# Optimization experiments

Measured on AMD Instinct MI355X. Metric: run time of the kernel, lower is better.

The kernel has to match this reference:

```python
import jax, jax.numpy as jnp
import numpy as np

C_IN = 512
C_MID = 256   # in_channels // ratio
ATTN_CH = 32  # SelectiveKernelAttn attn_channels
NUM_PATHS = 2
BN_EPS = 1e-5
LN_EPS = 1e-5


def conv1x1(x, w, b=None):
    # x: [B,C,H,W], w: [O,C] -> [B,O,H,W]
    y = jnp.einsum('oc,bchw->bohw', w, x)
    if b is not None:
        y = y + b[None, :, None, None]
    return y


def setup_inputs() -> dict:
    key = jax.random.key(0)
    ks = jax.random.split(key, 10)
    B, H, W = 16, 64, 64
    s = 0.05
    return {
        'x': jax.random.normal(ks[0], (B, C_IN, H, W), jnp.float32),
        # channel ('ch') branch params
        'w_qr': jax.random.normal(ks[1], (1, C_IN), jnp.float32) * s,
        'b_qr': jnp.zeros((1,), jnp.float32),
        'w_vr': jax.random.normal(ks[2], (C_MID, C_IN), jnp.float32) * s,
        'b_vr': jnp.zeros((C_MID,), jnp.float32),
        'w_up': jax.random.normal(ks[3], (C_IN, C_MID), jnp.float32) * s,
        'b_up': jnp.zeros((C_IN,), jnp.float32),
        'ln_g': jnp.ones((C_IN,), jnp.float32),
        'ln_b': jnp.zeros((C_IN,), jnp.float32),
        # spatial ('sp') branch params
        'w_ql': jax.random.normal(ks[4], (C_MID, C_IN), jnp.float32) * s,
        'b_ql': jnp.zeros((C_MID,), jnp.float32),
        'w_vl': jax.random.normal(ks[5], (C_MID, C_IN), jnp.float32) * s,
        'b_vl': jnp.zeros((C_MID,), jnp.float32),
        # SelectiveKernelAttn params (fc_reduce, bn eval stats, fc_select)
        'w_red': jax.random.normal(ks[6], (ATTN_CH, C_IN), jnp.float32) * s,
        'bn_g': jnp.ones((ATTN_CH,), jnp.float32),
        'bn_b': jnp.zeros((ATTN_CH,), jnp.float32),
        'bn_rm': jnp.zeros((ATTN_CH,), jnp.float32),
        'bn_rv': jnp.ones((ATTN_CH,), jnp.float32),
        'w_sel': jax.random.normal(ks[7], (C_IN * NUM_PATHS, ATTN_CH), jnp.float32) * s,
    }


def reference(x, w_qr, b_qr, w_vr, b_vr, w_up, b_up, ln_g, ln_b,
              w_ql, b_ql, w_vl, b_vl, w_red, bn_g, bn_b, bn_rm, bn_rv, w_sel):
    B, C, H, W = x.shape
    HW = H * W

    # ---- channel attention ('ch') ----
    input_x = conv1x1(x, w_vr, b_vr).reshape(B, C_MID, HW)            # [B,m,HW]
    mask = jax.nn.softmax(conv1x1(x, w_qr, b_qr).reshape(B, HW), axis=1)  # [B,HW]
    context = jnp.einsum('bmh,bh->bm', input_x, mask)                  # [B,m]
    up = jnp.einsum('om,bm->bo', w_up, context) + b_up                 # [B,C]
    mu = jnp.mean(up, axis=1, keepdims=True)
    var = jnp.var(up, axis=1, keepdims=True)
    ln = (up - mu) * jax.lax.rsqrt(var + LN_EPS) * ln_g + ln_b
    channel_attn = jax.nn.sigmoid(ln)                                  # [B,C]

    # ---- spatial attention ('sp') ----
    g_x = conv1x1(x, w_ql, b_ql)                                       # [B,m,H,W]
    avg = jax.nn.softmax(g_x.max(axis=(2, 3)), axis=1)                 # [B,m]
    theta = conv1x1(x, w_vl, b_vl).reshape(B, C_MID, HW)               # [B,m,HW]
    ctx = jnp.einsum('bm,bmh->bh', avg, theta)                         # [B,HW]
    spatial_attn = jax.nn.softmax(ctx, axis=1)                         # [B,HW]

    # ---- dsa fusion ----
    sequence = (channel_attn[:, :, None] * spatial_attn[:, None, :]).reshape(B, C, H, W)
    parallel = (channel_attn[:, :, None] + spatial_attn[:, None, :]).reshape(B, C, H, W)
    stack = jnp.stack([sequence, parallel], axis=1)                    # [B,2,C,H,W]

    # SelectiveKernelAttn (BN in eval mode with running stats)
    s = stack.sum(axis=1).mean(axis=(2, 3))                            # [B,C]
    red = jnp.einsum('ac,bc->ba', w_red, s)                            # [B,attn]
    red = (red - bn_rm) * jax.lax.rsqrt(bn_rv + BN_EPS) * bn_g + bn_b
    red = jax.nn.relu(red)
    sel = jnp.einsum('oa,ba->bo', w_sel, red).reshape(B, NUM_PATHS, C)
    sk_attn = jax.nn.softmax(sel, axis=1)                              # [B,2,C]

    sq_pr = (stack * sk_attn[:, :, :, None, None]).sum(axis=1)         # [B,C,H,W]
    return x * sq_pr + x
```

## Files before the change

kernel.cpp:

```cpp
#include <hip/hip_runtime.h>
#include <hip/hip_bf16.h>

#define BATCH 16
#define CIN   512
#define CMID  256
#define HWN   4096

typedef __bf16 bf16x8  __attribute__((ext_vector_type(8)));
typedef float  floatx4 __attribute__((ext_vector_type(4)));
typedef int    intx4   __attribute__((ext_vector_type(4)));

__device__ __forceinline__ unsigned short f2bf(float f){
  union { float f; unsigned int u; } v; v.f = f;
  unsigned int u = v.u;
  unsigned int r = u + 0x7FFFu + ((u >> 16) & 1u);
  return (unsigned short)(r >> 16);
}

__device__ __forceinline__ float wred(float v){
  #pragma unroll
  for (int o = 32; o >= 1; o >>= 1) v += __shfl_xor(v, o, 64);
  return v;
}

__device__ __forceinline__ float bsum(float v, float* scr, int t){
  v = wred(v);
  __syncthreads();
  if ((t & 63) == 0) scr[t >> 6] = v;
  __syncthreads();
  return scr[0] + scr[1] + scr[2] + scr[3];
}

__device__ __forceinline__ float bmax(float v, float* scr, int t){
  #pragma unroll
  for (int o = 32; o >= 1; o >>= 1) v = fmaxf(v, __shfl_xor(v, o, 64));
  __syncthreads();
  if ((t & 63) == 0) scr[t >> 6] = v;
  __syncthreads();
  return fmaxf(fmaxf(scr[0], scr[1]), fmaxf(scr[2], scr[3]));
}

__global__ __launch_bounds__(256) void k0_convert(const float* __restrict__ w,
                                                  unsigned short* __restrict__ wbf){
  int i = blockIdx.x * 256 + threadIdx.x;
  wbf[i] = f2bf(w[i]);
}

__global__ __launch_bounds__(256) void k1_gemm(
    const float* __restrict__ x, const unsigned short* __restrict__ wbf,
    const float* __restrict__ w_qr, float* __restrict__ qr, float* __restrict__ gpart)
{
  __shared__ __align__(16) unsigned short Blds[2][64 * 32];
  __shared__ float wqr_s[CIN];

  const int t = threadIdx.x;
  const int ntile = blockIdx.x, b = blockIdx.y;
  const int n0 = ntile * 64;
  const int lane = t & 63, wave = t >> 6, quad = lane >> 4, lm = lane & 15;
  const int n_own = t >> 2, q_own = t & 3;
  const int wblk = (n_own * 4 + (q_own ^ (n_own & 3))) * 8;

  wqr_s[t] = w_qr[t];
  wqr_s[t + 256] = w_qr[t + 256];
  __syncthreads();

  const float* xb = x + (size_t)b * CIN * HWN + (size_t)(q_own * 8) * HWN + n0 + n_own;

  floatx4 acc[4][4];
  #pragma unroll
  for (int i = 0; i < 4; ++i)
    #pragma unroll
    for (int jj = 0; jj < 4; ++jj)
      acc[i][jj] = (floatx4){0.f, 0.f, 0.f, 0.f};

  float qa = 0.f;
  float xv[8];
  bf16x8 afc[4], afn[4];

  #pragma unroll
  for (int j = 0; j < 8; ++j) xv[j] = xb[(size_t)j * HWN];
  #pragma unroll
  for (int j = 0; j < 8; ++j) qa = fmaf(wqr_s[q_own * 8 + j], xv[j], qa);
  {
    union { unsigned short u[8]; intx4 v; } pk;
    #pragma unroll
    for (int j = 0; j < 8; ++j) pk.u[j] = f2bf(xv[j]);
    *(intx4*)(&Blds[0][wblk]) = pk.v;
  }
  #pragma unroll
  for (int ms = 0; ms < 4; ++ms)
    afc[ms] = *(const bf16x8*)(&wbf[(size_t)(wave * 64 + ms * 16 + lm) * CIN + quad * 8]);
  __syncthreads();

  #pragma unroll 2
  for (int kt = 0; kt < 16; ++kt){
    const int cur = kt & 1;
    if (kt < 15){
      #pragma unroll
      for (int j = 0; j < 8; ++j) xv[j] = xb[(size_t)((kt + 1) * 32 + j) * HWN];
      #pragma unroll
      for (int ms = 0; ms < 4; ++ms)
        afn[ms] = *(const bf16x8*)(&wbf[(size_t)(wave * 64 + ms * 16 + lm) * CIN +
                                        (kt + 1) * 32 + quad * 8]);
    }
    bf16x8 bfr[4];
    #pragma unroll
    for (int ns = 0; ns < 4; ++ns){
      const int n = ns * 16 + lm;
      bfr[ns] = *(const bf16x8*)(&Blds[cur][(n * 4 + (quad ^ (n & 3))) * 8]);
    }
    #pragma unroll
    for (int ms = 0; ms < 4; ++ms)
      #pragma unroll
      for (int ns = 0; ns < 4; ++ns)
        acc[ms][ns] = __builtin_amdgcn_mfma_f32_16x16x32_bf16(afc[ms], bfr[ns], acc[ms][ns], 0, 0, 0);
    if (kt < 15){
      #pragma unroll
      for (int j = 0; j < 8; ++j)
        qa = fmaf(wqr_s[(kt + 1) * 32 + q_own * 8 + j], xv[j], qa);
      union { unsigned short u[8]; intx4 v; } pk;
      #pragma unroll
      for (int j = 0; j < 8; ++j) pk.u[j] = f2bf(xv[j]);
      *(intx4*)(&Blds[1 - cur][wblk]) = pk.v;
      #pragma unroll
      for (int ms = 0; ms < 4; ++ms) afc[ms] = afn[ms];
    }
    __syncthreads();
  }

  qa += __shfl_xor(qa, 1, 64);
  qa += __shfl_xor(qa, 2, 64);
  if ((t & 3) == 0) qr[b * HWN + n0 + n_own] = qa;

  #pragma unroll
  for (int ms = 0; ms < 4; ++ms){
    #pragma unroll
    for (int r = 0; r < 4; ++r){
      float v = fmaxf(fmaxf(acc[ms][0][r], acc[ms][1][r]),
                      fmaxf(acc[ms][2][r], acc[ms][3][r]));
      v = fmaxf(v, __shfl_xor(v, 1, 64));
      v = fmaxf(v, __shfl_xor(v, 2, 64));
      v = fmaxf(v, __shfl_xor(v, 4, 64));
      v = fmaxf(v, __shfl_xor(v, 8, 64));
      if ((lane & 15) == 0){
        const int m = wave * 64 + ms * 16 + (lane >> 4) * 4 + r;
        gpart[((b * 64 + ntile) * CMID) + m] = v;
      }
    }
  }
}

__global__ __launch_bounds__(256) void kr1_gmax(
    const float* __restrict__ gpart, const float* __restrict__ b_ql,
    float* __restrict__ gmax)
{
  __shared__ float part[8][32];
  const int b = blockIdx.x, g = blockIdx.y, t = threadIdx.x;
  const int m_l = t & 31, ng = t >> 5;
  const int m = g * 32 + m_l;
  float v = -3.0e38f;
  #pragma unroll
  for (int i = 0; i < 8; ++i)
    v = fmaxf(v, gpart[(size_t)(b * 64 + ng * 8 + i) * CMID + m]);
  part[ng][m_l] = v;
  __syncthreads();
  if (t < 32){
    float mx = part[0][t];
    #pragma unroll
    for (int i = 1; i < 8; ++i) mx = fmaxf(mx, part[i][t]);
    gmax[b * CMID + g * 32 + t] = mx + b_ql[g * 32 + t];
  }
}

__global__ __launch_bounds__(256) void kr2_prep(
    const float* __restrict__ gmax, const float* __restrict__ w_vl,
    const float* __restrict__ qr,
    float* __restrict__ wmix, float* __restrict__ stats,
    float* __restrict__ xmask, float* __restrict__ ctx)
{
  __shared__ float scr[4];
  __shared__ float avg_s[CMID];
  __shared__ float wsum[2][128];
  const int b = blockIdx.x, cg = blockIdx.y, t = threadIdx.x;

  if (cg < 4){
    ((floatx4*)(ctx + (size_t)b * HWN + cg * 1024))[t] = (floatx4){0.f,0.f,0.f,0.f};

    float gv = gmax[b * CMID + t];
    float mx = bmax(gv, scr, t);
    float e = expf(gv - mx);
    float s = bsum(e, scr, t);
    avg_s[t] = e / s;
    __syncthreads();

    const int c = cg * 128 + (t & 127);
    const int half = t >> 7;
    float acc = 0.f;
    #pragma unroll 8
    for (int mi = 0; mi < 128; ++mi){
      const int m = half * 128 + mi;
      acc = fmaf(w_vl[(size_t)m * CIN + c], avg_s[m], acc);
    }
    wsum[half][t & 127] = acc;
    __syncthreads();
    if (t < 128) wmix[b * CIN + cg * 128 + t] = wsum[0][t] + wsum[1][t];
  } else {
    xmask[b * CIN + t] = 0.f;
    xmask[b * CIN + t + 256] = 0.f;
    const float* qb = qr + (size_t)b * HWN;
    float qm = -3.0e38f;
    #pragma unroll
    for (int i = 0; i < 16; ++i) qm = fmaxf(qm, qb[t + i * 256]);
    qm = bmax(qm, scr, t);
    float qs = 0.f;
    #pragma unroll
    for (int i = 0; i < 16; ++i) qs += expf(qb[t + i * 256] - qm);
    qs = bsum(qs, scr, t);
    if (t == 0){ stats[b] = qm; stats[16 + b] = qs; }
  }
}

__global__ __launch_bounds__(256) void k3_dual(
    const float* __restrict__ x, const float* __restrict__ qr,
    const float* __restrict__ stats, const float* __restrict__ wmix,
    float* __restrict__ xmask, float* __restrict__ ctx)
{
  const int ht = blockIdx.x, ct = blockIdx.y, b = blockIdx.z;
  const int t = threadIdx.x;
  const int j = t & 15, i = t >> 4;
  const int c0 = ct * 128, h0 = ht * 128;
  const float* xb = x + (size_t)b * CIN * HWN;
  const float qm = stats[b], inv_qs = 1.0f / stats[16 + b];

  floatx4 maskv[2];
  #pragma unroll
  for (int l = 0; l < 2; ++l)
    #pragma unroll
    for (int d = 0; d < 4; ++d)
      maskv[l][d] = expf(qr[b*HWN + h0 + j*4 + d + 64*l] - qm) * inv_qs;

  float wmv[8];
  #pragma unroll
  for (int k = 0; k < 8; ++k)
    wmv[k] = wmix[b*CIN + c0 + i + 16*k];

  float xm[8] = {0,0,0,0,0,0,0,0};
  floatx4 cx[2];
  cx[0] = (floatx4){0.f,0.f,0.f,0.f};
  cx[1] = (floatx4){0.f,0.f,0.f,0.f};

  #pragma unroll
  for (int k = 0; k < 8; ++k){
    const float* row = xb + (size_t)(c0 + i + 16*k) * HWN + h0 + j*4;
    floatx4 v0 = *(const floatx4*)(row);
    floatx4 v1 = *(const floatx4*)(row + 64);
    floatx4 p = v0 * maskv[0] + v1 * maskv[1];
    xm[k] = (p[0] + p[1]) + (p[2] + p[3]);
    cx[0] += v0 * wmv[k];
    cx[1] += v1 * wmv[k];
  }

  #pragma unroll
  for (int k = 0; k < 8; ++k){
    float v = xm[k];
    v += __shfl_xor(v, 1, 64); v += __shfl_xor(v, 2, 64);
    v += __shfl_xor(v, 4, 64); v += __shfl_xor(v, 8, 64);
    if (j == 0) atomicAdd(&xmask[b*CIN + c0 + i + 16*k], v);
  }
  #pragma unroll
  for (int l = 0; l < 2; ++l)
    #pragma unroll
    for (int d = 0; d < 4; ++d){
      float v = cx[l][d];
      v += __shfl_xor(v, 16, 64); v += __shfl_xor(v, 32, 64);
      if (((t & 63) >> 4) == 0) atomicAdd(&ctx[b*HWN + h0 + j*4 + d + 64*l], v);
    }
}

__global__ __launch_bounds__(256) void kr4_context(
    const float* __restrict__ xmask, const float* __restrict__ w_vr,
    const float* __restrict__ b_vr, float* __restrict__ ctxm)
{
  __shared__ __align__(16) float xm_s[CIN];
  const int b = blockIdx.x, half = blockIdx.y, t = threadIdx.x;
  const int kl = t & 15, rg = t >> 4;

  xm_s[t] = xmask[b * CIN + t];
  xm_s[t + 256] = xmask[b * CIN + t + 256];
  __syncthreads();

  floatx4 xf[8];
  #pragma unroll
  for (int jf = 0; jf < 8; ++jf)
    xf[jf] = *(const floatx4*)(&xm_s[(jf * 16 + kl) * 4]);

  #pragma unroll
  for (int pass = 0; pass < 8; ++pass){
    const int m = half * 128 + pass * 16 + rg;
    const floatx4* wr = (const floatx4*)(w_vr + (size_t)m * CIN);
    floatx4 pacc = (floatx4){0.f,0.f,0.f,0.f};
    #pragma unroll
    for (int jf = 0; jf < 8; ++jf)
      pacc += wr[jf * 16 + kl] * xf[jf];
    float acc = (pacc[0] + pacc[1]) + (pacc[2] + pacc[3]);
    acc += __shfl_xor(acc, 1, 64); acc += __shfl_xor(acc, 2, 64);
    acc += __shfl_xor(acc, 4, 64); acc += __shfl_xor(acc, 8, 64);
    if (kl == 0) ctxm[b * CMID + m] = acc + b_vr[m];
  }
}

__global__ __launch_bounds__(256) void kr5_tail(
    const float* __restrict__ ctxm, const float* __restrict__ w_up, const float* __restrict__ b_up,
    const float* __restrict__ ln_g, const float* __restrict__ ln_b,
    const float* __restrict__ w_red, const float* __restrict__ bn_g, const float* __restrict__ bn_b,
    const float* __restrict__ bn_rm, const float* __restrict__ bn_rv,
    const float* __restrict__ w_sel, const float* __restrict__ ctxg,
    float* __restrict__ P, float* __restrict__ Q, float* __restrict__ sp)
{
  __shared__ float scr[4];
  __shared__ __align__(16) float cm_s[CMID];
  __shared__ __align__(16) float up_s[CIN];
  __shared__ __align__(16) float ch_s[CIN];
  __shared__ float red_s[32];
  const int b = blockIdx.x, t = threadIdx.x;

  cm_s[t] = ctxm[b * CMID + t];
  __syncthreads();

  {
    const int kl = t & 7;
    floatx4 cf[8];
    #pragma unroll
    for (int jf = 0; jf < 8; ++jf)
      cf[jf] = *(const floatx4*)(&cm_s[(jf * 8 + kl) * 4]);
    #pragma unroll
    for (int pass = 0; pass < 16; ++pass){
      const int o = pass * 32 + (t >> 3);
      const floatx4* wr = (const floatx4*)(w_up + (size_t)o * CMID);
      floatx4 pacc = (floatx4){0.f,0.f,0.f,0.f};
      #pragma unroll
      for (int jf = 0; jf < 8; ++jf)
        pacc += wr[jf * 8 + kl] * cf[jf];
      float acc = (pacc[0] + pacc[1]) + (pacc[2] + pacc[3]);
      acc += __shfl_xor(acc, 1, 64); acc += __shfl_xor(acc, 2, 64);
      acc += __shfl_xor(acc, 4, 64);
      if (kl == 0) up_s[o] = acc + b_up[o];
    }
  }
  __syncthreads();

  float up0 = up_s[t], up1 = up_s[t + 256];
  float mu = bsum(up0 + up1, scr, t) * (1.0f / 512.0f);
  float d0 = up0 - mu, d1 = up1 - mu;
  float var = bsum(d0*d0 + d1*d1, scr, t) * (1.0f / 512.0f);
  float rstd = rsqrtf(var + 1e-5f);
  float ch0 = 1.f / (1.f + expf(-(d0 * rstd * ln_g[t] + ln_b[t])));
  float ch1 = 1.f / (1.f + expf(-(d1 * rstd * ln_g[t + 256] + ln_b[t + 256])));
  ch_s[t] = ch0; ch_s[t + 256] = ch1;
  __syncthreads();

  {
    const int kl = t & 7, a = t >> 3;
    const float k1 = 1.0f + 1.0f/4096.0f, k2 = 1.0f/4096.0f;
    const floatx4* wrd = (const floatx4*)(w_red + (size_t)a * CIN);
    float racc = 0.f;
    #pragma unroll
    for (int jf = 0; jf < 16; ++jf){
      floatx4 wv = wrd[jf * 8 + kl];
      floatx4 cv = *(const floatx4*)(&ch_s[(jf * 8 + kl) * 4]);
      racc += wv[0] * fmaf(cv[0], k1, k2) + wv[1] * fmaf(cv[1], k1, k2)
            + wv[2] * fmaf(cv[2], k1, k2) + wv[3] * fmaf(cv[3], k1, k2);
    }
    racc += __shfl_xor(racc, 1, 64); racc += __shfl_xor(racc, 2, 64);
    racc += __shfl_xor(racc, 4, 64);
    if (kl == 0){
      float bn = (racc - bn_rm[a]) * rsqrtf(bn_rv[a] + 1e-5f) * bn_g[a] + bn_b[a];
      red_s[a] = fmaxf(bn, 0.0f);
    }
  }
  __syncthreads();

  #pragma unroll
  for (int q = 0; q < 2; ++q){
    const int c = t + q * 256;
    const floatx4* ws0 = (const floatx4*)(w_sel + (size_t)c * 32);
    const floatx4* ws1 = (const floatx4*)(w_sel + (size_t)(CIN + c) * 32);
    float s0 = 0.f, s1 = 0.f;
    #pragma unroll
    for (int a4 = 0; a4 < 8; ++a4){
      floatx4 w0 = ws0[a4], w1 = ws1[a4];
      #pragma unroll
      for (int d = 0; d < 4; ++d){
        float r = red_s[a4 * 4 + d];
        s0 = fmaf(w0[d], r, s0);
        s1 = fmaf(w1[d], r, s1);
      }
    }
    float a0 = 1.f / (1.f + expf(s1 - s0));
    float a1 = 1.f - a0;
    float ch = ch_s[c];
    P[b*CIN + c] = 1.0f + a1 * ch;
    Q[b*CIN + c] = a0 * ch + a1;
  }

  const float* cb = ctxg + (size_t)b * HWN;
  float cm = -3.0e38f;
  #pragma unroll
  for (int i = 0; i < 16; ++i) cm = fmaxf(cm, cb[t + i * 256]);
  cm = bmax(cm, scr, t);
  float cs = 0.f;
  float ev[16];
  #pragma unroll
  for (int i = 0; i < 16; ++i){ ev[i] = expf(cb[t + i * 256] - cm); cs += ev[i]; }
  cs = bsum(cs, scr, t);
  const float inv = 1.0f / cs;
  #pragma unroll
  for (int i = 0; i < 16; ++i) sp[b*HWN + t + i * 256] = ev[i] * inv;
}

__global__ __launch_bounds__(256) void k5_out(
    const float* __restrict__ x, const float* __restrict__ P, const float* __restrict__ Q,
    const float* __restrict__ sp, float* __restrict__ out)
{
  const int bc = blockIdx.x;
  const int b = bc >> 9;
  const int t = threadIdx.x;
  const float p = P[bc], q = Q[bc];
  const floatx4* xr = (const floatx4*)(x + (size_t)bc * HWN);
  const floatx4* sr = (const floatx4*)(sp + (size_t)b * HWN);
  floatx4* outr = (floatx4*)(out + (size_t)bc * HWN);
  #pragma unroll
  for (int r = 0; r < 4; ++r){
    const int idx = t + r * 256;
    floatx4 xv = xr[idx];
    floatx4 sv = sr[idx];
    outr[idx] = xv * (p + sv * q);
  }
}

extern "C" void kernel_launch(void* const* d_in, const int* in_sizes, int n_in,
                              void* d_out, int out_size, void* d_ws, size_t ws_size,
                              hipStream_t stream)
{
  (void)in_sizes; (void)n_in; (void)out_size; (void)ws_size;
  const float* x    = (const float*)d_in[0];
  const float* w_qr = (const float*)d_in[1];
  const float* w_vr = (const float*)d_in[3];
  const float* b_vr = (const float*)d_in[4];
  const float* w_up = (const float*)d_in[5];
  const float* b_up = (const float*)d_in[6];
  const float* ln_g = (const float*)d_in[7];
  const float* ln_b = (const float*)d_in[8];
  const float* w_ql = (const float*)d_in[9];
  const float* b_ql = (const float*)d_in[10];
  const float* w_vl = (const float*)d_in[11];
  const float* w_red = (const float*)d_in[13];
  const float* bn_g  = (const float*)d_in[14];
  const float* bn_b  = (const float*)d_in[15];
  const float* bn_rm = (const float*)d_in[16];
  const float* bn_rv = (const float*)d_in[17];
  const float* w_sel = (const float*)d_in[18];
  float* out = (float*)d_out;

  char* ws = (char*)d_ws;
  unsigned short* wbf = (unsigned short*)(ws + 0);
  float* qr    = (float*)(ws + 262144);
  float* gpart = (float*)(ws + 524288);
  float* wmix  = (float*)(ws + 1572864);
  float* xmask = (float*)(ws + 1605632);
  float* ctx   = (float*)(ws + 1638400);
  float* sp    = (float*)(ws + 1900544);
  float* P     = (float*)(ws + 2162688);
  float* Q     = (float*)(ws + 2195456);
  float* stats = (float*)(ws + 2228224);
  float* gmax  = (float*)(ws + 2228352);
  float* ctxm  = (float*)(ws + 2244736);

  k0_convert<<<512, 256, 0, stream>>>(w_ql, wbf);
  k1_gemm<<<dim3(64, BATCH), 256, 0, stream>>>(x, wbf, w_qr, qr, gpart);
  kr1_gmax<<<dim3(BATCH, 8), 256, 0, stream>>>(gpart, b_ql, gmax);
  kr2_prep<<<dim3(BATCH, 5), 256, 0, stream>>>(gmax, w_vl, qr, wmix, stats, xmask, ctx);
  k3_dual<<<dim3(32, 4, BATCH), 256, 0, stream>>>(x, qr, stats, wmix, xmask, ctx);
  kr4_context<<<dim3(BATCH, 2), 256, 0, stream>>>(xmask, w_vr, b_vr, ctxm);
  kr5_tail<<<BATCH, 256, 0, stream>>>(ctxm, w_up, b_up, ln_g, ln_b,
                                      w_red, bn_g, bn_b, bn_rm, bn_rv, w_sel, ctx,
                                      P, Q, sp);
  k5_out<<<BATCH * CIN, 256, 0, stream>>>(x, P, Q, sp, out);
}
```

Before: 395.4 us.

## Remap thread-to-data ownership in GEMM loads and dual-reduction kernel for coalescing

In the GEMM kernel, each wave now loads a contiguous 64-pixel row segment per channel group instead of 4 threads sharing a pixel, so global x loads become fully coalesced; the qr partial sums are then combined through shared memory. The dual reduction kernel is restructured so each wave handles 16 channels across 256 contiguous pixels with float4 loads, reducing the mask-weighted sum with a full wave reduction and the ctx sum across waves in shared memory before fewer atomics. This trades some extra shared memory and a barrier for better memory access patterns and reduced atomic traffic on the bandwidth-bound passes over x.

```diff
diff --git a/kernel.cpp b/kernel.cpp
--- a/kernel.cpp
+++ b/kernel.cpp
@@ -52,19 +52,21 @@
 {
   __shared__ __align__(16) unsigned short Blds[2][64 * 32];
   __shared__ float wqr_s[CIN];
+  __shared__ float qp[4][64];
 
   const int t = threadIdx.x;
   const int ntile = blockIdx.x, b = blockIdx.y;
   const int n0 = ntile * 64;
   const int lane = t & 63, wave = t >> 6, quad = lane >> 4, lm = lane & 15;
-  const int n_own = t >> 2, q_own = t & 3;
-  const int wblk = (n_own * 4 + (q_own ^ (n_own & 3))) * 8;
+  const int n_own = t & 63;
+  const int ko    = wave;
+  const int wblk = (n_own * 4 + (ko ^ (n_own & 3))) * 8;
 
   wqr_s[t] = w_qr[t];
   wqr_s[t + 256] = w_qr[t + 256];
   __syncthreads();
 
-  const float* xb = x + (size_t)b * CIN * HWN + (size_t)(q_own * 8) * HWN + n0 + n_own;
+  const float* xb = x + (size_t)b * CIN * HWN + (size_t)(ko * 8) * HWN + n0 + n_own;
 
   floatx4 acc[4][4];
   #pragma unroll
@@ -80,7 +82,7 @@
   #pragma unroll
   for (int j = 0; j < 8; ++j) xv[j] = xb[(size_t)j * HWN];
   #pragma unroll
-  for (int j = 0; j < 8; ++j) qa = fmaf(wqr_s[q_own * 8 + j], xv[j], qa);
+  for (int j = 0; j < 8; ++j) qa = fmaf(wqr_s[ko * 8 + j], xv[j], qa);
   {
     union { unsigned short u[8]; intx4 v; } pk;
     #pragma unroll
@@ -117,7 +119,7 @@
     if (kt < 15){
       #pragma unroll
       for (int j = 0; j < 8; ++j)
-        qa = fmaf(wqr_s[(kt + 1) * 32 + q_own * 8 + j], xv[j], qa);
+        qa = fmaf(wqr_s[(kt + 1) * 32 + ko * 8 + j], xv[j], qa);
       union { unsigned short u[8]; intx4 v; } pk;
       #pragma unroll
       for (int j = 0; j < 8; ++j) pk.u[j] = f2bf(xv[j]);
@@ -128,9 +130,9 @@
     __syncthreads();
   }
 
-  qa += __shfl_xor(qa, 1, 64);
-  qa += __shfl_xor(qa, 2, 64);
-  if ((t & 3) == 0) qr[b * HWN + n0 + n_own] = qa;
+  qp[wave][lane] = qa;
+  __syncthreads();
+  if (t < 64) qr[b * HWN + n0 + t] = qp[0][t] + qp[1][t] + qp[2][t] + qp[3][t];
 
   #pragma unroll
   for (int ms = 0; ms < 4; ++ms){
@@ -225,56 +227,50 @@
     const float* __restrict__ stats, const float* __restrict__ wmix,
     float* __restrict__ xmask, float* __restrict__ ctx)
 {
-  const int ht = blockIdx.x, ct = blockIdx.y, b = blockIdx.z;
+  __shared__ floatx4 cxs[4][64];
+  const int hwt = blockIdx.x, ct = blockIdx.y, b = blockIdx.z;
   const int t = threadIdx.x;
-  const int j = t & 15, i = t >> 4;
-  const int c0 = ct * 128, h0 = ht * 128;
-  const float* xb = x + (size_t)b * CIN * HWN;
+  const int lane = t & 63, wave = t >> 6;
+  const int c0 = ct * 64 + wave * 16;
+  const int hw0 = hwt * 256;
   const float qm = stats[b], inv_qs = 1.0f / stats[16 + b];
 
-  floatx4 maskv[2];
-  #pragma unroll
-  for (int l = 0; l < 2; ++l)
+  floatx4 maskv;
+  {
+    const float* qb = qr + (size_t)b * HWN + hw0 + lane * 4;
+    #pragma unroll
+    for (int d = 0; d < 4; ++d) maskv[d] = expf(qb[d] - qm) * inv_qs;
+  }
+
+  float wmv[16];
+  #pragma unroll
+  for (int r = 0; r < 16; ++r) wmv[r] = wmix[b*CIN + c0 + r];
+
+  const float* xr0 = x + (size_t)b * CIN * HWN + (size_t)c0 * HWN + hw0 + lane * 4;
+
+  floatx4 xv[16];
+  #pragma unroll
+  for (int r = 0; r < 16; ++r) xv[r] = *(const floatx4*)(xr0 + (size_t)r * HWN);
+
+  floatx4 cx = (floatx4){0.f,0.f,0.f,0.f};
+  #pragma unroll
+  for (int r = 0; r < 16; ++r) cx += xv[r] * wmv[r];
+
+  #pragma unroll
+  for (int r = 0; r < 16; ++r){
+    floatx4 p = xv[r] * maskv;
+    float v = wred((p[0] + p[1]) + (p[2] + p[3]));
+    if (lane == 0) atomicAdd(&xmask[b*CIN + c0 + r], v);
+  }
+
+  cxs[wave][lane] = cx;
+  __syncthreads();
+  if (t < 64){
+    floatx4 s = cxs[0][t] + cxs[1][t] + cxs[2][t] + cxs[3][t];
     #pragma unroll
     for (int d = 0; d < 4; ++d)
-      maskv[l][d] = expf(qr[b*HWN + h0 + j*4 + d + 64*l] - qm) * inv_qs;
-
-  float wmv[8];
-  #pragma unroll
-  for (int k = 0; k < 8; ++k)
-    wmv[k] = wmix[b*CIN + c0 + i + 16*k];
-
-  float xm[8] = {0,0,0,0,0,0,0,0};
-  floatx4 cx[2];
-  cx[0] = (floatx4){0.f,0.f,0.f,0.f};
-  cx[1] = (floatx4){0.f,0.f,0.f,0.f};
-
-  #pragma unroll
-  for (int k = 0; k < 8; ++k){
-    const float* row = xb + (size_t)(c0 + i + 16*k) * HWN + h0 + j*4;
-    floatx4 v0 = *(const floatx4*)(row);
-    floatx4 v1 = *(const floatx4*)(row + 64);
-    floatx4 p = v0 * maskv[0] + v1 * maskv[1];
-    xm[k] = (p[0] + p[1]) + (p[2] + p[3]);
-    cx[0] += v0 * wmv[k];
-    cx[1] += v1 * wmv[k];
-  }
-
-  #pragma unroll
-  for (int k = 0; k < 8; ++k){
-    float v = xm[k];
-    v += __shfl_xor(v, 1, 64); v += __shfl_xor(v, 2, 64);
-    v += __shfl_xor(v, 4, 64); v += __shfl_xor(v, 8, 64);
-    if (j == 0) atomicAdd(&xmask[b*CIN + c0 + i + 16*k], v);
-  }
-  #pragma unroll
-  for (int l = 0; l < 2; ++l)
-    #pragma unroll
-    for (int d = 0; d < 4; ++d){
-      float v = cx[l][d];
-      v += __shfl_xor(v, 16, 64); v += __shfl_xor(v, 32, 64);
-      if (((t & 63) >> 4) == 0) atomicAdd(&ctx[b*HWN + h0 + j*4 + d + 64*l], v);
-    }
+      atomicAdd(&ctx[b*HWN + hw0 + t*4 + d], s[d]);
+  }
 }
 
 __global__ __launch_bounds__(256) void kr4_context(
@@ -480,7 +476,7 @@
   k1_gemm<<<dim3(64, BATCH), 256, 0, stream>>>(x, wbf, w_qr, qr, gpart);
   kr1_gmax<<<dim3(BATCH, 8), 256, 0, stream>>>(gpart, b_ql, gmax);
   kr2_prep<<<dim3(BATCH, 5), 256, 0, stream>>>(gmax, w_vl, qr, wmix, stats, xmask, ctx);
-  k3_dual<<<dim3(32, 4, BATCH), 256, 0, stream>>>(x, qr, stats, wmix, xmask, ctx);
+  k3_dual<<<dim3(16, 8, BATCH), 256, 0, stream>>>(x, qr, stats, wmix, xmask, ctx);
   kr4_context<<<dim3(BATCH, 2), 256, 0, stream>>>(xmask, w_vr, b_vr, ctxm);
   kr5_tail<<<BATCH, 256, 0, stream>>>(ctxm, w_up, b_up, ln_g, ln_b,
                                       w_red, bn_g, bn_b, bn_rm, bn_rv, w_sel, ctx,
```

Result: no change. 390.5 us (-1.2%).
